# Optimization experiments

Measured on AMD Instinct MI355X. Metric: run time of the kernel, lower is better.

## Reference

```python
import jax, jax.numpy as jnp
import numpy as np

N_NODES = 50000


def _segment_softmax(alpha, dst, num_segments):
    # alpha: [E, H] edge attention logits, softmax-normalized per destination node
    m = jax.ops.segment_max(alpha, dst, num_segments=num_segments)
    m = jnp.where(jnp.isfinite(m), m, 0.0)
    e = jnp.exp(alpha - m[dst])
    s = jax.ops.segment_sum(e, dst, num_segments=num_segments)
    return e / (s[dst] + 1e-16)


def _gat_layer(x, W, att_src, att_dst, bias, src, dst, heads, ch, concat):
    N = x.shape[0]
    xp = (x @ W).reshape(N, heads, ch)                      # [N, H, C]
    a_s = jnp.einsum('nhc,hc->nh', xp, att_src)              # [N, H]
    a_d = jnp.einsum('nhc,hc->nh', xp, att_dst)              # [N, H]
    alpha = jax.nn.leaky_relu(a_s[src] + a_d[dst], 0.2)      # [E, H]
    alpha = _segment_softmax(alpha, dst, N)
    out = jax.ops.segment_sum(alpha[:, :, None] * xp[src], dst, num_segments=N)  # [N, H, C]
    out = out.reshape(N, heads * ch) if concat else out.mean(axis=1)
    return out + bias


def setup_inputs() -> dict:
    key = jax.random.key(0)
    ks = jax.random.split(key, 10)
    IN, HID, HEADS, OUT, E = 128, 64, 4, 32, 640000
    x = jax.random.normal(ks[0], (N_NODES, IN), jnp.float32)
    edge_index = jax.random.randint(ks[1], (2, E), 0, N_NODES, dtype=jnp.int32)
    W1 = jax.random.normal(ks[2], (IN, HEADS * HID), jnp.float32) * (1.0 / np.sqrt(IN))
    att_src1 = jax.random.normal(ks[3], (HEADS, HID), jnp.float32) * 0.1
    att_dst1 = jax.random.normal(ks[4], (HEADS, HID), jnp.float32) * 0.1
    b1 = jnp.zeros((HEADS * HID,), jnp.float32)
    W2 = jax.random.normal(ks[5], (HEADS * HID, OUT), jnp.float32) * (1.0 / np.sqrt(HEADS * HID))
    att_src2 = jax.random.normal(ks[6], (1, OUT), jnp.float32) * 0.1
    att_dst2 = jax.random.normal(ks[7], (1, OUT), jnp.float32) * 0.1
    b2 = jnp.zeros((OUT,), jnp.float32)
    return {"x": x, "edge_index": edge_index, "W1": W1, "att_src1": att_src1,
            "att_dst1": att_dst1, "b1": b1, "W2": W2, "att_src2": att_src2,
            "att_dst2": att_dst2, "b2": b2}


def reference(x, edge_index, W1, att_src1, att_dst1, b1, W2, att_src2, att_dst2, b2):
    N = x.shape[0]
    # PyG GATConv default: add self-loops
    loop = jnp.arange(N, dtype=edge_index.dtype)
    src = jnp.concatenate([edge_index[0], loop])
    dst = jnp.concatenate([edge_index[1], loop])
    HID = att_src1.shape[1]
    HEADS = att_src1.shape[0]
    OUT = att_src2.shape[1]
    # dropout layers are identity in eval mode
    h = jax.nn.elu(_gat_layer(x, W1, att_src1, att_dst1, b1, src, dst, HEADS, HID, True))
    out = _gat_layer(h, W2, att_src2, att_dst2, b2, src, dst, 1, OUT, False)
    return jax.nn.softmax(out, axis=1)
```

## Files before the change

kernel.cpp:

```cpp
#include <hip/hip_runtime.h>
#include <math.h>
#include <stdint.h>

#define NEG_SENT -1e30f

typedef __attribute__((ext_vector_type(8))) short bf16x8;
typedef __attribute__((ext_vector_type(4))) float f32x4;

__device__ __forceinline__ unsigned short f2bf(float f) {
    unsigned u = __float_as_uint(f);
    unsigned r = u + 0x7FFFu + ((u >> 16) & 1u);
    return (unsigned short)(r >> 16);
}
__device__ __forceinline__ float bf2f(unsigned short h) {
    return __uint_as_float(((unsigned)h) << 16);
}

__global__ __launch_bounds__(256) void prep_count(const float* __restrict__ w1,
        const float* __restrict__ w2, unsigned short* __restrict__ w1t,
        unsigned short* __restrict__ w2t, const int* __restrict__ ei,
        int E, int Etot, int* __restrict__ deg) {
    int b = blockIdx.x;
    if (b < 160) {
        int tidx = b * 256 + threadIdx.x;
        if (b < 128) {
            int k = tidx & 127, n = tidx >> 7;
            w1t[tidx] = f2bf(w1[k * 256 + n]);
        } else {
            int idx = tidx - 32768;
            int k = idx & 255, n = idx >> 8;
            w2t[idx] = f2bf(w2[k * 32 + n]);
        }
    } else {
        int e = (b - 160) * 256 + threadIdx.x;
        if (e >= Etot) return;
        int d = (e < E) ? ei[E + e] : e - E;
        atomicAdd(&deg[d], 1);
    }
}

__global__ __launch_bounds__(256) void gemm1_mfma(
        const float* __restrict__ x,
        const unsigned short* __restrict__ w1t,
        const float* __restrict__ att_s, const float* __restrict__ att_d,
        unsigned short* __restrict__ xph,
        float* __restrict__ a_s, float* __restrict__ a_d, int M) {
    int wave = (int)(((long)blockIdx.x * 256 + threadIdx.x) >> 6);
    int lane = threadIdx.x & 63;
    int row0 = wave * 16;
    if (row0 >= M) return;
    int r = lane & 15;
    int g = lane >> 4;
    bf16x8 a[4];
    const float* arow = x + (long)(row0 + r) * 128 + g * 8;
    #pragma unroll
    for (int k0 = 0; k0 < 4; ++k0) {
        float4 f0 = *(const float4*)(arow + k0 * 32);
        float4 f1 = *(const float4*)(arow + k0 * 32 + 4);
        bf16x8 af;
        af[0] = (short)f2bf(f0.x); af[1] = (short)f2bf(f0.y);
        af[2] = (short)f2bf(f0.z); af[3] = (short)f2bf(f0.w);
        af[4] = (short)f2bf(f1.x); af[5] = (short)f2bf(f1.y);
        af[6] = (short)f2bf(f1.z); af[7] = (short)f2bf(f1.w);
        a[k0] = af;
    }
    float as_v[16], ad_v[16];
    #pragma unroll
    for (int nt = 0; nt < 16; ++nt) {
        as_v[nt] = att_s[nt * 16 + r];
        ad_v[nt] = att_d[nt * 16 + r];
    }
    f32x4 acc[16];
    #pragma unroll
    for (int nt = 0; nt < 16; ++nt) acc[nt] = (f32x4){0.f, 0.f, 0.f, 0.f};
    #pragma unroll
    for (int nt = 0; nt < 16; ++nt) {
        const unsigned short* brow = w1t + (long)(nt * 16 + r) * 128 + g * 8;
        #pragma unroll
        for (int k0 = 0; k0 < 4; ++k0) {
            bf16x8 b = *(const bf16x8*)(brow + k0 * 32);
            acc[nt] = __builtin_amdgcn_mfma_f32_16x16x32_bf16(a[k0], b, acc[nt], 0, 0, 0);
        }
    }
    float ps[4][4] = {};
    float pd[4][4] = {};
    #pragma unroll
    for (int nt = 0; nt < 16; ++nt) {
        int hh = nt >> 2;
        #pragma unroll
        for (int q = 0; q < 4; ++q) {
            float v = acc[nt][q];
            xph[(long)(row0 + g * 4 + q) * 256 + nt * 16 + r] = f2bf(v);
            ps[q][hh] += v * as_v[nt];
            pd[q][hh] += v * ad_v[nt];
        }
    }
    #pragma unroll
    for (int off = 1; off < 16; off <<= 1) {
        #pragma unroll
        for (int q = 0; q < 4; ++q)
            #pragma unroll
            for (int hh = 0; hh < 4; ++hh) {
                ps[q][hh] += __shfl_xor(ps[q][hh], off);
                pd[q][hh] += __shfl_xor(pd[q][hh], off);
            }
    }
    if (r == 0) {
        #pragma unroll
        for (int q = 0; q < 4; ++q) {
            int row = row0 + g * 4 + q;
            #pragma unroll
            for (int hh = 0; hh < 4; ++hh) {
                a_s[row * 4 + hh] = ps[q][hh];
                a_d[row * 4 + hh] = pd[q][hh];
            }
        }
    }
}

__global__ __launch_bounds__(256) void gemm2_mfma(
        const unsigned short* __restrict__ hb,
        const unsigned short* __restrict__ w2t,
        const float* __restrict__ att_s, const float* __restrict__ att_d,
        unsigned short* __restrict__ xp2h,
        float* __restrict__ a_s, float* __restrict__ a_d, int M) {
    int wave = (int)(((long)blockIdx.x * 256 + threadIdx.x) >> 6);
    int lane = threadIdx.x & 63;
    int row0 = wave * 16;
    if (row0 >= M) return;
    int r = lane & 15;
    int g = lane >> 4;
    bf16x8 a[8];
    const unsigned short* arow = hb + (long)(row0 + r) * 256 + g * 8;
    #pragma unroll
    for (int k0 = 0; k0 < 8; ++k0)
        a[k0] = *(const bf16x8*)(arow + k0 * 32);
    float as_v[2], ad_v[2];
    #pragma unroll
    for (int nt = 0; nt < 2; ++nt) {
        as_v[nt] = att_s[nt * 16 + r];
        ad_v[nt] = att_d[nt * 16 + r];
    }
    f32x4 acc[2];
    acc[0] = (f32x4){0.f, 0.f, 0.f, 0.f};
    acc[1] = (f32x4){0.f, 0.f, 0.f, 0.f};
    #pragma unroll
    for (int nt = 0; nt < 2; ++nt) {
        const unsigned short* brow = w2t + (long)(nt * 16 + r) * 256 + g * 8;
        #pragma unroll
        for (int k0 = 0; k0 < 8; ++k0) {
            bf16x8 b = *(const bf16x8*)(brow + k0 * 32);
            acc[nt] = __builtin_amdgcn_mfma_f32_16x16x32_bf16(a[k0], b, acc[nt], 0, 0, 0);
        }
    }
    float ps[4] = {}, pd[4] = {};
    #pragma unroll
    for (int nt = 0; nt < 2; ++nt) {
        #pragma unroll
        for (int q = 0; q < 4; ++q) {
            float v = acc[nt][q];
            xp2h[(long)(row0 + g * 4 + q) * 32 + nt * 16 + r] = f2bf(v);
            ps[q] += v * as_v[nt];
            pd[q] += v * ad_v[nt];
        }
    }
    #pragma unroll
    for (int off = 1; off < 16; off <<= 1) {
        #pragma unroll
        for (int q = 0; q < 4; ++q) {
            ps[q] += __shfl_xor(ps[q], off);
            pd[q] += __shfl_xor(pd[q], off);
        }
    }
    if (r == 0) {
        #pragma unroll
        for (int q = 0; q < 4; ++q) {
            a_s[row0 + g * 4 + q] = ps[q];
            a_d[row0 + g * 4 + q] = pd[q];
        }
    }
}

__global__ __launch_bounds__(256) void scan_local(const int* __restrict__ deg,
        int* __restrict__ rowptr, int* __restrict__ blocksum, int N) {
    __shared__ int part[256];
    int b = blockIdx.x, t = threadIdx.x;
    int base = b * 1024 + t * 4;
    int4 v = make_int4(0, 0, 0, 0);
    if (base + 3 < N) {
        v = *(const int4*)(deg + base);
    } else {
        if (base + 0 < N) v.x = deg[base + 0];
        if (base + 1 < N) v.y = deg[base + 1];
        if (base + 2 < N) v.z = deg[base + 2];
        if (base + 3 < N) v.w = deg[base + 3];
    }
    part[t] = v.x + v.y + v.z + v.w;
    __syncthreads();
    #pragma unroll
    for (int off = 1; off < 256; off <<= 1) {
        int val = (t >= off) ? part[t - off] : 0;
        __syncthreads();
        part[t] += val;
        __syncthreads();
    }
    if (t == 255) blocksum[b] = part[255];
    int r0 = (t > 0) ? part[t - 1] : 0;
    int r1 = r0 + v.x;
    int r2 = r1 + v.y;
    int r3 = r2 + v.z;
    if (base + 3 < N) {
        *(int4*)(rowptr + base) = make_int4(r0, r1, r2, r3);
    } else {
        if (base + 0 < N) rowptr[base + 0] = r0;
        if (base + 1 < N) rowptr[base + 1] = r1;
        if (base + 2 < N) rowptr[base + 2] = r2;
        if (base + 3 < N) rowptr[base + 3] = r3;
    }
}

__global__ __launch_bounds__(256) void scan_add(int* __restrict__ rowptr,
        const int* __restrict__ blocksum, int* __restrict__ cursor,
        int N, int Etot, int nb) {
    __shared__ int part[256];
    int b = blockIdx.x, t = threadIdx.x;
    part[t] = (t < nb) ? blocksum[t] : 0;
    __syncthreads();
    #pragma unroll
    for (int off = 1; off < 256; off <<= 1) {
        int val = (t >= off) ? part[t - off] : 0;
        __syncthreads();
        part[t] += val;
        __syncthreads();
    }
    int off_b = (b > 0) ? part[b - 1] : 0;
    int base = b * 1024 + t * 4;
    if (base + 3 < N) {
        int4 v = *(const int4*)(rowptr + base);
        v.x += off_b; v.y += off_b; v.z += off_b; v.w += off_b;
        *(int4*)(rowptr + base) = v;
        *(int4*)(cursor + base) = v;
    } else {
        for (int i = 0; i < 4; ++i) {
            if (base + i < N) {
                int v = rowptr[base + i] + off_b;
                rowptr[base + i] = v;
                cursor[base + i] = v;
            }
        }
    }
    if (b == 0 && t == 0) rowptr[N] = Etot;
}

__global__ __launch_bounds__(256) void scatter_edges(const int* __restrict__ ei,
        int E, int Etot, int* __restrict__ cursor, int* __restrict__ csr_src) {
    int e = blockIdx.x * 256 + threadIdx.x;
    if (e >= Etot) return;
    int s, d;
    if (e < E) { s = ei[e]; d = ei[E + e]; } else { s = e - E; d = s; }
    int pos = atomicAdd(&cursor[d], 1);
    csr_src[pos] = s;
}

__global__ __launch_bounds__(256) void sort_rows(const int* __restrict__ rowptr,
        int* __restrict__ csr_src, int N) {
    __shared__ int buf[4][256];
    __shared__ int mxw[4];
    int t = threadIdx.x;
    int w = t >> 6;
    int lane = t & 63;
    int d = blockIdx.x * 4 + w;
    int row0 = 0, deg = 0;
    if (d < N) { row0 = rowptr[d]; deg = rowptr[d + 1] - row0; }
    int capped = (deg <= 256) ? deg : 0;
    for (int j = lane; j < capped; j += 64) buf[w][j] = csr_src[row0 + j];
    int m = capped;
    #pragma unroll
    for (int off = 32; off; off >>= 1) m = max(m, __shfl_xor(m, off));
    if (lane == 0) mxw[w] = m;
    __syncthreads();
    int itmax = max(max(mxw[0], mxw[1]), max(mxw[2], mxw[3]));
    for (int it = 0; it < itmax; ++it) {
        int start = it & 1;
        #pragma unroll
        for (int rep = 0; rep < 2; ++rep) {
            int k = start + 2 * lane + rep * 128;
            if (k + 1 < capped) {
                int a = buf[w][k], b = buf[w][k + 1];
                if (a > b) { buf[w][k] = b; buf[w][k + 1] = a; }
            }
        }
        __syncthreads();
    }
    for (int j = lane; j < capped; j += 64) csr_src[row0 + j] = buf[w][j];
    if (deg > 256 && lane == 0) {
        for (int i = 1; i < deg; ++i) {
            int key = csr_src[row0 + i];
            int k = i - 1;
            while (k >= 0 && csr_src[row0 + k] > key) {
                csr_src[row0 + k + 1] = csr_src[row0 + k];
                --k;
            }
            csr_src[row0 + k + 1] = key;
        }
    }
}

__device__ __forceinline__ void merge_ms(float& m, float& s, float m2, float s2) {
    float mn = fmaxf(m, m2);
    s = s * expf(m - mn) + s2 * expf(m2 - mn);
    m = mn;
}

__global__ __launch_bounds__(256) void agg1_fused(const int* __restrict__ rowptr,
        const int* __restrict__ csr_src, const float* __restrict__ a_s,
        const float* __restrict__ a_d, const ushort4* __restrict__ xph4,
        const float* __restrict__ bias, ushort4* __restrict__ hb4, int N) {
    __shared__ unsigned short cbuf[4][1024];
    int t = threadIdx.x;
    int w = t >> 6;
    int lane = t & 63;
    int d = blockIdx.x * 4 + w;
    bool active = d < N;
    int row0 = 0, deg = 0;
    if (active) { row0 = rowptr[d]; deg = rowptr[d + 1] - row0; }
    int h = lane & 3;
    int j0 = lane >> 2;
    float ad = active ? a_d[d * 4 + h] : 0.f;
    float m = NEG_SENT, s = 0.f;
    for (int j = j0; j < deg; j += 16) {
        int sn = csr_src[row0 + j];
        float l = a_s[sn * 4 + h] + ad;
        l = l > 0.f ? l : 0.2f * l;
        float mn = fmaxf(m, l);
        s = s * expf(m - mn) + expf(l - mn);
        m = mn;
    }
    #pragma unroll
    for (int off = 4; off <= 32; off <<= 1) {
        float m2 = __shfl_xor(m, off);
        float s2 = __shfl_xor(s, off);
        merge_ms(m, s, m2, s2);
    }
    float inv = 1.f / (s + 1e-16f);
    int cap = deg < 256 ? deg : 256;
    for (int j = j0; j < cap; j += 16) {
        int sn = csr_src[row0 + j];
        float l = a_s[sn * 4 + h] + ad;
        l = l > 0.f ? l : 0.2f * l;
        cbuf[w][j * 4 + h] = f2bf(expf(l - m) * inv);
    }
    __syncthreads();
    if (!active) return;
    int hsel = lane >> 4;
    float m_h   = __shfl(m, hsel);
    float inv_h = __shfl(inv, hsel);
    float ad_h  = __shfl(ad, hsel);
    float4 acc = make_float4(0.f, 0.f, 0.f, 0.f);
    int j = 0;
    for (; j + 4 <= cap; j += 4) {
        long e0 = row0 + j;
        int s0 = csr_src[e0 + 0];
        int s1 = csr_src[e0 + 1];
        int s2 = csr_src[e0 + 2];
        int s3 = csr_src[e0 + 3];
        float c0 = bf2f(cbuf[w][(j + 0) * 4 + hsel]);
        float c1 = bf2f(cbuf[w][(j + 1) * 4 + hsel]);
        float c2 = bf2f(cbuf[w][(j + 2) * 4 + hsel]);
        float c3 = bf2f(cbuf[w][(j + 3) * 4 + hsel]);
        ushort4 u0 = xph4[(long)s0 * 64 + lane];
        ushort4 u1 = xph4[(long)s1 * 64 + lane];
        ushort4 u2 = xph4[(long)s2 * 64 + lane];
        ushort4 u3 = xph4[(long)s3 * 64 + lane];
        acc.x += c0 * bf2f(u0.x); acc.y += c0 * bf2f(u0.y);
        acc.z += c0 * bf2f(u0.z); acc.w += c0 * bf2f(u0.w);
        acc.x += c1 * bf2f(u1.x); acc.y += c1 * bf2f(u1.y);
        acc.z += c1 * bf2f(u1.z); acc.w += c1 * bf2f(u1.w);
        acc.x += c2 * bf2f(u2.x); acc.y += c2 * bf2f(u2.y);
        acc.z += c2 * bf2f(u2.z); acc.w += c2 * bf2f(u2.w);
        acc.x += c3 * bf2f(u3.x); acc.y += c3 * bf2f(u3.y);
        acc.z += c3 * bf2f(u3.z); acc.w += c3 * bf2f(u3.w);
    }
    for (; j < deg; ++j) {
        long e = row0 + j;
        int sn = csr_src[e];
        float c;
        if (j < 256) {
            c = bf2f(cbuf[w][j * 4 + hsel]);
        } else {
            float l = a_s[sn * 4 + hsel] + ad_h;
            l = l > 0.f ? l : 0.2f * l;
            c = bf2f(f2bf(expf(l - m_h) * inv_h));
        }
        ushort4 u = xph4[(long)sn * 64 + lane];
        acc.x += c * bf2f(u.x); acc.y += c * bf2f(u.y);
        acc.z += c * bf2f(u.z); acc.w += c * bf2f(u.w);
    }
    float4 b = ((const float4*)bias)[lane];
    float vx = acc.x + b.x; vx = vx > 0.f ? vx : expm1f(vx);
    float vy = acc.y + b.y; vy = vy > 0.f ? vy : expm1f(vy);
    float vz = acc.z + b.z; vz = vz > 0.f ? vz : expm1f(vz);
    float vw = acc.w + b.w; vw = vw > 0.f ? vw : expm1f(vw);
    ushort4 o;
    o.x = f2bf(vx); o.y = f2bf(vy); o.z = f2bf(vz); o.w = f2bf(vw);
    hb4[(long)d * 64 + lane] = o;
}

__global__ __launch_bounds__(256) void agg2_fused(const int* __restrict__ rowptr,
        const int* __restrict__ csr_src, const float* __restrict__ a_s,
        const float* __restrict__ a_d, const unsigned short* __restrict__ xp2h,
        const float* __restrict__ bias, float* __restrict__ out, int N) {
    int t = threadIdx.x;
    int d = blockIdx.x * 8 + (t >> 5);
    if (d >= N) return;
    int c = t & 31;
    int row0 = rowptr[d];
    int deg = rowptr[d + 1] - row0;
    float ad = a_d[d];
    float m = NEG_SENT, s = 0.f;
    for (int j = c; j < deg; j += 32) {
        int sn = csr_src[row0 + j];
        float l = a_s[sn] + ad;
        l = l > 0.f ? l : 0.2f * l;
        float mn = fmaxf(m, l);
        s = s * expf(m - mn) + expf(l - mn);
        m = mn;
    }
    #pragma unroll
    for (int off = 1; off <= 16; off <<= 1) {
        float m2 = __shfl_xor(m, off, 32);
        float s2 = __shfl_xor(s, off, 32);
        merge_ms(m, s, m2, s2);
    }
    float inv = 1.f / (s + 1e-16f);
    float acc = 0.f;
    int j = 0;
    for (; j + 4 <= deg; j += 4) {
        long e0 = row0 + j;
        int s0 = csr_src[e0 + 0];
        int s1 = csr_src[e0 + 1];
        int s2 = csr_src[e0 + 2];
        int s3 = csr_src[e0 + 3];
        float l0 = a_s[s0] + ad; l0 = l0 > 0.f ? l0 : 0.2f * l0;
        float l1 = a_s[s1] + ad; l1 = l1 > 0.f ? l1 : 0.2f * l1;
        float l2 = a_s[s2] + ad; l2 = l2 > 0.f ? l2 : 0.2f * l2;
        float l3 = a_s[s3] + ad; l3 = l3 > 0.f ? l3 : 0.2f * l3;
        float c0 = expf(l0 - m) * inv;
        float c1 = expf(l1 - m) * inv;
        float c2 = expf(l2 - m) * inv;
        float c3 = expf(l3 - m) * inv;
        float v0 = bf2f(xp2h[(long)s0 * 32 + c]);
        float v1 = bf2f(xp2h[(long)s1 * 32 + c]);
        float v2 = bf2f(xp2h[(long)s2 * 32 + c]);
        float v3 = bf2f(xp2h[(long)s3 * 32 + c]);
        acc += c0 * v0;
        acc += c1 * v1;
        acc += c2 * v2;
        acc += c3 * v3;
    }
    for (; j < deg; ++j) {
        long e = row0 + j;
        int sn = csr_src[e];
        float l = a_s[sn] + ad; l = l > 0.f ? l : 0.2f * l;
        float co = expf(l - m) * inv;
        acc += co * bf2f(xp2h[(long)sn * 32 + c]);
    }
    float v = acc + bias[c];
    float mx = v;
    #pragma unroll
    for (int off = 16; off; off >>= 1) mx = fmaxf(mx, __shfl_xor(mx, off, 32));
    float ex = expf(v - mx);
    float sm = ex;
    #pragma unroll
    for (int off = 16; off; off >>= 1) sm += __shfl_xor(sm, off, 32);
    out[(long)d * 32 + c] = ex / sm;
}

extern "C" void kernel_launch(void* const* d_in, const int* in_sizes, int n_in,
                              void* d_out, int out_size, void* d_ws, size_t ws_size,
                              hipStream_t stream) {
    const float* x   = (const float*)d_in[0];
    const int*   ei  = (const int*)d_in[1];
    const float* W1  = (const float*)d_in[2];
    const float* as1 = (const float*)d_in[3];
    const float* ad1 = (const float*)d_in[4];
    const float* b1  = (const float*)d_in[5];
    const float* W2  = (const float*)d_in[6];
    const float* as2 = (const float*)d_in[7];
    const float* ad2 = (const float*)d_in[8];
    const float* b2  = (const float*)d_in[9];
    float* out = (float*)d_out;

    const int N = in_sizes[0] / 128;
    const int E = in_sizes[1] / 2;
    const int Etot = E + N;

    unsigned short* xp1h = (unsigned short*)d_ws;
    unsigned short* hb   = xp1h + (long)N * 256;
    unsigned short* w1t  = hb + (long)N * 256;
    unsigned short* w2t  = w1t + 32768;
    unsigned short* xp2h = w2t + 8192;
    float* a_s1   = (float*)(xp2h + (long)N * 32);
    float* a_d1   = a_s1 + (long)N * 4;
    float* a_s2   = a_d1 + (long)N * 4;
    float* a_d2   = a_s2 + N;
    int* deg      = (int*)(a_d2 + N);
    int* rowptr   = deg + N;
    int* cursor   = rowptr + N + 4;
    int* csr_src  = cursor + N;
    int* blocksum = csr_src + Etot;

    hipMemsetAsync(deg, 0, (size_t)N * sizeof(int), stream);

    int nbE = (Etot + 255) / 256;
    int nbS = (N + 1023) / 1024;
    prep_count<<<160 + nbE, 256, 0, stream>>>(W1, W2, w1t, w2t, ei, E, Etot, deg);
    scan_local<<<nbS, 256, 0, stream>>>(deg, rowptr, blocksum, N);
    scan_add<<<nbS, 256, 0, stream>>>(rowptr, blocksum, cursor, N, Etot, nbS);
    scatter_edges<<<nbE, 256, 0, stream>>>(ei, E, Etot, cursor, csr_src);
    sort_rows<<<(N + 3) / 4, 256, 0, stream>>>(rowptr, csr_src, N);

    int gemmBlocks = (((N + 15) / 16) + 3) / 4;

    gemm1_mfma<<<gemmBlocks, 256, 0, stream>>>(x, w1t, as1, ad1,
                                               xp1h, a_s1, a_d1, N);
    agg1_fused<<<(N + 3) / 4, 256, 0, stream>>>(rowptr, csr_src, a_s1, a_d1,
                                                (const ushort4*)xp1h, b1,
                                                (ushort4*)hb, N);

    gemm2_mfma<<<gemmBlocks, 256, 0, stream>>>(hb, w2t, as2, ad2,
                                               xp2h, a_s2, a_d2, N);
    agg2_fused<<<(N + 7) / 8, 256, 0, stream>>>(rowptr, csr_src, a_s2, a_d2,
                                                xp2h, b2, out, N);
}
```

Measured before the change: 258.3 us.

## Restructure edge softmax into two-pass LDS-cached form and drop block barriers

The online max/sum softmax with its shuffle-merge is replaced in both aggregation kernels by a max pass that caches leaky-relu logits in shared memory, then a sum pass that stores unnormalized exponentials. Normalization by the sum is applied once to the accumulated output instead of per edge. In agg2, per-edge a_s gathers and exps in the main loop are replaced by bf16 coefficients from shared memory. Block-level __syncthreads are removed from sort_rows and agg1, and sort_rows now loops to each wave's own degree; this relies on each wave touching only its own shared buffer. Extra shared memory may reduce occupancy, and the bf16 coefficients in agg2 slightly change rounding.

```diff
diff --git a/kernel.cpp b/kernel.cpp
--- a/kernel.cpp
+++ b/kernel.cpp
@@ -265,7 +265,6 @@
 __global__ __launch_bounds__(256) void sort_rows(const int* __restrict__ rowptr,
         int* __restrict__ csr_src, int N) {
     __shared__ int buf[4][256];
-    __shared__ int mxw[4];
     int t = threadIdx.x;
     int w = t >> 6;
     int lane = t & 63;
@@ -274,13 +273,7 @@
     if (d < N) { row0 = rowptr[d]; deg = rowptr[d + 1] - row0; }
     int capped = (deg <= 256) ? deg : 0;
     for (int j = lane; j < capped; j += 64) buf[w][j] = csr_src[row0 + j];
-    int m = capped;
-    #pragma unroll
-    for (int off = 32; off; off >>= 1) m = max(m, __shfl_xor(m, off));
-    if (lane == 0) mxw[w] = m;
-    __syncthreads();
-    int itmax = max(max(mxw[0], mxw[1]), max(mxw[2], mxw[3]));
-    for (int it = 0; it < itmax; ++it) {
+    for (int it = 0; it < capped; ++it) {
         int start = it & 1;
         #pragma unroll
         for (int rep = 0; rep < 2; ++rep) {
@@ -290,7 +283,6 @@
                 if (a > b) { buf[w][k] = b; buf[w][k + 1] = a; }
             }
         }
-        __syncthreads();
     }
     for (int j = lane; j < capped; j += 64) csr_src[row0 + j] = buf[w][j];
     if (deg > 256 && lane == 0) {
@@ -306,16 +298,11 @@
     }
 }
 
-__device__ __forceinline__ void merge_ms(float& m, float& s, float m2, float s2) {
-    float mn = fmaxf(m, m2);
-    s = s * expf(m - mn) + s2 * expf(m2 - mn);
-    m = mn;
-}
-
 __global__ __launch_bounds__(256) void agg1_fused(const int* __restrict__ rowptr,
         const int* __restrict__ csr_src, const float* __restrict__ a_s,
         const float* __restrict__ a_d, const ushort4* __restrict__ xph4,
         const float* __restrict__ bias, ushort4* __restrict__ hb4, int N) {
+    __shared__ float lbuf[4][1024];
     __shared__ unsigned short cbuf[4][1024];
     int t = threadIdx.x;
     int w = t >> 6;
@@ -327,35 +314,39 @@
     int h = lane & 3;
     int j0 = lane >> 2;
     float ad = active ? a_d[d * 4 + h] : 0.f;
-    float m = NEG_SENT, s = 0.f;
+    float m = NEG_SENT;
     for (int j = j0; j < deg; j += 16) {
         int sn = csr_src[row0 + j];
         float l = a_s[sn * 4 + h] + ad;
         l = l > 0.f ? l : 0.2f * l;
-        float mn = fmaxf(m, l);
-        s = s * expf(m - mn) + expf(l - mn);
-        m = mn;
-    }
-    #pragma unroll
-    for (int off = 4; off <= 32; off <<= 1) {
-        float m2 = __shfl_xor(m, off);
-        float s2 = __shfl_xor(s, off);
-        merge_ms(m, s, m2, s2);
-    }
+        if (j < 256) lbuf[w][j * 4 + h] = l;
+        m = fmaxf(m, l);
+    }
+    #pragma unroll
+    for (int off = 4; off <= 32; off <<= 1) m = fmaxf(m, __shfl_xor(m, off));
+    float s = 0.f;
+    for (int j = j0; j < deg; j += 16) {
+        float l;
+        if (j < 256) {
+            l = lbuf[w][j * 4 + h];
+        } else {
+            int sn = csr_src[row0 + j];
+            l = a_s[sn * 4 + h] + ad;
+            l = l > 0.f ? l : 0.2f * l;
+        }
+        float e = expf(l - m);
+        if (j < 256) cbuf[w][j * 4 + h] = f2bf(e);
+        s += e;
+    }
+    #pragma unroll
+    for (int off = 4; off <= 32; off <<= 1) s += __shfl_xor(s, off);
     float inv = 1.f / (s + 1e-16f);
-    int cap = deg < 256 ? deg : 256;
-    for (int j = j0; j < cap; j += 16) {
-        int sn = csr_src[row0 + j];
-        float l = a_s[sn * 4 + h] + ad;
-        l = l > 0.f ? l : 0.2f * l;
-        cbuf[w][j * 4 + h] = f2bf(expf(l - m) * inv);
-    }
-    __syncthreads();
     if (!active) return;
     int hsel = lane >> 4;
     float m_h   = __shfl(m, hsel);
     float inv_h = __shfl(inv, hsel);
     float ad_h  = __shfl(ad, hsel);
+    int cap = deg < 256 ? deg : 256;
     float4 acc = make_float4(0.f, 0.f, 0.f, 0.f);
     int j = 0;
     for (; j + 4 <= cap; j += 4) {
@@ -390,17 +381,17 @@
         } else {
             float l = a_s[sn * 4 + hsel] + ad_h;
             l = l > 0.f ? l : 0.2f * l;
-            c = bf2f(f2bf(expf(l - m_h) * inv_h));
+            c = bf2f(f2bf(expf(l - m_h)));
         }
         ushort4 u = xph4[(long)sn * 64 + lane];
         acc.x += c * bf2f(u.x); acc.y += c * bf2f(u.y);
         acc.z += c * bf2f(u.z); acc.w += c * bf2f(u.w);
     }
     float4 b = ((const float4*)bias)[lane];
-    float vx = acc.x + b.x; vx = vx > 0.f ? vx : expm1f(vx);
-    float vy = acc.y + b.y; vy = vy > 0.f ? vy : expm1f(vy);
-    float vz = acc.z + b.z; vz = vz > 0.f ? vz : expm1f(vz);
-    float vw = acc.w + b.w; vw = vw > 0.f ? vw : expm1f(vw);
+    float vx = acc.x * inv_h + b.x; vx = vx > 0.f ? vx : expm1f(vx);
+    float vy = acc.y * inv_h + b.y; vy = vy > 0.f ? vy : expm1f(vy);
+    float vz = acc.z * inv_h + b.z; vz = vz > 0.f ? vz : expm1f(vz);
+    float vw = acc.w * inv_h + b.w; vw = vw > 0.f ? vw : expm1f(vw);
     ushort4 o;
     o.x = f2bf(vx); o.y = f2bf(vy); o.z = f2bf(vz); o.w = f2bf(vw);
     hb4[(long)d * 64 + lane] = o;
@@ -410,45 +401,56 @@
         const int* __restrict__ csr_src, const float* __restrict__ a_s,
         const float* __restrict__ a_d, const unsigned short* __restrict__ xp2h,
         const float* __restrict__ bias, float* __restrict__ out, int N) {
+    __shared__ float lbuf[8][256];
+    __shared__ unsigned short ebuf[8][256];
     int t = threadIdx.x;
-    int d = blockIdx.x * 8 + (t >> 5);
+    int w2 = t >> 5;
+    int d = blockIdx.x * 8 + w2;
     if (d >= N) return;
     int c = t & 31;
     int row0 = rowptr[d];
     int deg = rowptr[d + 1] - row0;
     float ad = a_d[d];
-    float m = NEG_SENT, s = 0.f;
+    float m = NEG_SENT;
     for (int j = c; j < deg; j += 32) {
         int sn = csr_src[row0 + j];
         float l = a_s[sn] + ad;
         l = l > 0.f ? l : 0.2f * l;
-        float mn = fmaxf(m, l);
-        s = s * expf(m - mn) + expf(l - mn);
-        m = mn;
-    }
-    #pragma unroll
-    for (int off = 1; off <= 16; off <<= 1) {
-        float m2 = __shfl_xor(m, off, 32);
-        float s2 = __shfl_xor(s, off, 32);
-        merge_ms(m, s, m2, s2);
-    }
+        if (j < 256) lbuf[w2][j] = l;
+        m = fmaxf(m, l);
+    }
+    #pragma unroll
+    for (int off = 1; off <= 16; off <<= 1) m = fmaxf(m, __shfl_xor(m, off, 32));
+    float s = 0.f;
+    for (int j = c; j < deg; j += 32) {
+        float l;
+        if (j < 256) {
+            l = lbuf[w2][j];
+        } else {
+            int sn = csr_src[row0 + j];
+            l = a_s[sn] + ad;
+            l = l > 0.f ? l : 0.2f * l;
+        }
+        float e = expf(l - m);
+        if (j < 256) ebuf[w2][j] = f2bf(e);
+        s += e;
+    }
+    #pragma unroll
+    for (int off = 1; off <= 16; off <<= 1) s += __shfl_xor(s, off, 32);
     float inv = 1.f / (s + 1e-16f);
+    int cap = deg < 256 ? deg : 256;
     float acc = 0.f;
     int j = 0;
-    for (; j + 4 <= deg; j += 4) {
+    for (; j + 4 <= cap; j += 4) {
         long e0 = row0 + j;
         int s0 = csr_src[e0 + 0];
         int s1 = csr_src[e0 + 1];
         int s2 = csr_src[e0 + 2];
         int s3 = csr_src[e0 + 3];
-        float l0 = a_s[s0] + ad; l0 = l0 > 0.f ? l0 : 0.2f * l0;
-        float l1 = a_s[s1] + ad; l1 = l1 > 0.f ? l1 : 0.2f * l1;
-        float l2 = a_s[s2] + ad; l2 = l2 > 0.f ? l2 : 0.2f * l2;
-        float l3 = a_s[s3] + ad; l3 = l3 > 0.f ? l3 : 0.2f * l3;
-        float c0 = expf(l0 - m) * inv;
-        float c1 = expf(l1 - m) * inv;
-        float c2 = expf(l2 - m) * inv;
-        float c3 = expf(l3 - m) * inv;
+        float c0 = bf2f(ebuf[w2][j + 0]);
+        float c1 = bf2f(ebuf[w2][j + 1]);
+        float c2 = bf2f(ebuf[w2][j + 2]);
+        float c3 = bf2f(ebuf[w2][j + 3]);
         float v0 = bf2f(xp2h[(long)s0 * 32 + c]);
         float v1 = bf2f(xp2h[(long)s1 * 32 + c]);
         float v2 = bf2f(xp2h[(long)s2 * 32 + c]);
@@ -461,11 +463,16 @@
     for (; j < deg; ++j) {
         long e = row0 + j;
         int sn = csr_src[e];
-        float l = a_s[sn] + ad; l = l > 0.f ? l : 0.2f * l;
-        float co = expf(l - m) * inv;
+        float co;
+        if (j < 256) {
+            co = bf2f(ebuf[w2][j]);
+        } else {
+            float l = a_s[sn] + ad; l = l > 0.f ? l : 0.2f * l;
+            co = bf2f(f2bf(expf(l - m)));
+        }
         acc += co * bf2f(xp2h[(long)sn * 32 + c]);
     }
-    float v = acc + bias[c];
+    float v = acc * inv + bias[c];
     float mx = v;
     #pragma unroll
     for (int off = 16; off; off >>= 1) mx = fmaxf(mx, __shfl_xor(mx, off, 32));
```

Result: faster. 246.7 us (-4.5%).
